# Kernel optimization log

Hardware: AMD Instinct MI355X
Metric: run time of the kernel (lower is better)

## Reference

```python
import jax, jax.numpy as jnp
import numpy as np

B, T = 64, 256
STOCH, DETER = 1024, 4096
D = 512          # attention_dim == embed_dim == heads*dim_head
H, HD = 8, 64    # heads, dim_head
FF = 2 * D       # feedforward hidden
L = 2            # transformer layers
NT = 255         # embedding rows (len(targets))
OUT = 255        # np.prod(shape)
SCALE = HD ** -0.5
EPS = 1e-5


def _ln(x, g, b):
    m = jnp.mean(x, axis=-1, keepdims=True)
    v = jnp.mean((x - m) ** 2, axis=-1, keepdims=True)
    return (x - m) * jax.lax.rsqrt(v + EPS) * g + b


def setup_inputs() -> dict:
    key = jax.random.key(0)
    ks = jax.random.split(key, 32)
    r = lambda i, shp, s=0.02: (jax.random.normal(ks[i], shp, dtype=jnp.float32) * s)
    inp = {
        'stoch': jax.random.normal(ks[0], (B, T, STOCH), dtype=jnp.float32),
        'deter': jax.random.normal(ks[1], (B, T, DETER), dtype=jnp.float32),
        'targets_array': jax.random.randint(ks[2], (B, T), 0, NT),
        'emb': r(3, (NT, D), 1.0),
        'Ws': r(4, (D, STOCH)), 'bs': jnp.zeros((D,), jnp.float32),
        'Wd': r(5, (D, DETER)), 'bd': jnp.zeros((D,), jnp.float32),
        # per-layer stacked params [L, ...]
        'ln1_g': jnp.ones((L, D), jnp.float32), 'ln1_b': jnp.zeros((L, D), jnp.float32),
        'Wqkv': r(6, (L, 3 * H * HD, D)),
        'Wout': r(7, (L, D, H * HD)), 'bout': jnp.zeros((L, D), jnp.float32),
        'ln2_g': jnp.ones((L, D), jnp.float32), 'ln2_b': jnp.zeros((L, D), jnp.float32),
        'W1': r(8, (L, FF, D)), 'b1': jnp.zeros((L, FF), jnp.float32),
        'W2': r(9, (L, D, FF)), 'b2': jnp.zeros((L, D), jnp.float32),
        'W1b': r(10, (L, FF, D)), 'b1b': jnp.zeros((L, FF), jnp.float32),
        'W2b': r(11, (L, D, FF)), 'b2b': jnp.zeros((L, D), jnp.float32),
        'Wm': r(12, (OUT, D)), 'bm': jnp.zeros((OUT,), jnp.float32),
    }
    return inp


def _forward(stoch, deter, targets_array, emb, Ws, bs, Wd, bd,
             ln1_g, ln1_b, Wqkv, Wout, bout, ln2_g, ln2_b,
             W1, b1, W2, b2, W1b, b1b, W2b, b2b, Wm, bm):
    N = B * T
    s = stoch.reshape(N, STOCH)
    d = deter.reshape(N, DETER)
    tg = targets_array.reshape(N)
    tok1 = (s @ Ws.T + bs)[:, None, :]   # [N,1,D]
    tok2 = (d @ Wd.T + bd)[:, None, :]
    x = jnp.concatenate([tok1, tok2], axis=1)   # [N,2,D]
    q2 = emb[tg][:, None, :]                    # [N,1,D]

    for l in range(L):
        # PreNorm -> Attention (residuals connect to the normalized inputs,
        # exactly as in the original code)
        xn = _ln(x, ln1_g[l], ln1_b[l])
        qn = _ln(q2, ln1_g[l], ln1_b[l])
        qkv = xn @ Wqkv[l].T                            # [N,2,3*H*HD]
        q, k, v = jnp.split(qkv, 3, axis=-1)
        q = q.reshape(N, 2, H, HD).transpose(0, 2, 1, 3)   # [N,H,2,HD]
        k = k.reshape(N, 2, H, HD).transpose(0, 2, 1, 3)
        v = v.reshape(N, 2, H, HD).transpose(0, 2, 1, 3)
        qq2 = qn.reshape(N, 1, H, HD).transpose(0, 2, 1, 3)  # [N,H,1,HD]
        dots = jnp.einsum('nhqd,nhkd->nhqk', q, k) * SCALE
        dots2 = jnp.einsum('nhqd,nhkd->nhqk', qq2, k) * SCALE
        attn = jax.nn.log_softmax(dots, axis=-1)    # LogSoftmax attention!
        attn2 = jax.nn.log_softmax(dots2, axis=-1)
        out = jnp.einsum('nhqk,nhkd->nhqd', attn, v).transpose(0, 2, 1, 3).reshape(N, 2, H * HD)
        qout = jnp.einsum('nhqk,nhkd->nhqd', attn2, v).transpose(0, 2, 1, 3).reshape(N, 1, H * HD)
        x = out @ Wout[l].T + bout[l] + xn   # to_out on self stream only
        q2 = qout + qn                        # cross stream has NO projection

        # PreNorm -> FeedForward (dual streams, separate MLPs, exact GELU)
        xn = _ln(x, ln2_g[l], ln2_b[l])
        qn = _ln(q2, ln2_g[l], ln2_b[l])
        x = jax.nn.gelu(xn @ W1[l].T + b1[l], approximate=False) @ W2[l].T + b2[l] + xn
        q2 = jax.nn.gelu(qn @ W1b[l].T + b1b[l], approximate=False) @ W2b[l].T + b2b[l] + qn

    out = q2.reshape(B, T, D)
    mean = out @ Wm.T + bm   # [B,T,OUT]
    return mean


def reference(stoch, deter, targets_array, emb, Ws, bs, Wd, bd,
              ln1_g, ln1_b, Wqkv, Wout, bout, ln2_g, ln2_b,
              W1, b1, W2, b2, W1b, b1b, W2b, b2b, Wm, bm):
    return _forward(stoch, deter, targets_array, emb, Ws, bs, Wd, bd,
                    ln1_g, ln1_b, Wqkv, Wout, bout, ln2_g, ln2_b,
                    W1, b1, W2, b2, W1b, b1b, W2b, b2b, Wm, bm)
```

## Files before the change

### kernel.cpp

```cpp
#include <hip/hip_runtime.h>
#include <cstdint>
#include <cstddef>


#define NTOK   16384
#define TWO_N  32768
#define DMODEL 512
#define HEADS  8
#define HDIM   64
#define FFDIM  1024
#define KSTOCH 1024
#define KDETER 4096
#define QKVD   1536
#define NOUT   255

typedef short bf16x8 __attribute__((ext_vector_type(8)));
typedef float f32x4  __attribute__((ext_vector_type(4)));

__device__ inline unsigned short bfbits(float f) {
  union { float f; unsigned u; } x; x.f = f;
  unsigned r = x.u + 0x7fffu + ((x.u >> 16) & 1u);
  return (unsigned short)(r >> 16);
}
__device__ inline float bf2f(unsigned short s) {
  union { unsigned u; float f; } x; x.u = ((unsigned)s) << 16;
  return x.f;
}
__device__ inline float wave_sum(float v) {
  #pragma unroll
  for (int o = 32; o > 0; o >>= 1) v += __shfl_xor(v, o);
  return v;
}

struct CvtEnt { const float* src; unsigned short* dst; int n4; int ntot4; };
struct CvtArgs { CvtEnt e[11]; };

__global__ __launch_bounds__(256) void cvt_kernel(CvtArgs args) {
  CvtEnt ent = args.e[blockIdx.y];
  int stride = gridDim.x * 256;
  for (int i = blockIdx.x * 256 + threadIdx.x; i < ent.ntot4; i += stride) {
    float4 v;
    if (i < ent.n4) v = ((const float4*)ent.src)[i];
    else            v = make_float4(0.f, 0.f, 0.f, 0.f);
    ushort4 o;
    o.x = bfbits(v.x); o.y = bfbits(v.y); o.z = bfbits(v.z); o.w = bfbits(v.w);
    ((ushort4*)ent.dst)[i] = o;
  }
}

__global__ __launch_bounds__(128) void gather_kernel(
    const float* __restrict__ emb, const int* __restrict__ tg,
    float* __restrict__ q2) {
  int n = blockIdx.x;
  int row = tg[n];
  ((float4*)(q2 + (size_t)n * DMODEL))[threadIdx.x] =
      ((const float4*)(emb + (size_t)row * DMODEL))[threadIdx.x];
}

__global__ __launch_bounds__(256) void ln_kernel(
    const float* __restrict__ x, const float* __restrict__ g,
    const float* __restrict__ b, float* __restrict__ of,
    unsigned short* __restrict__ ob, int rows) {
  int w = threadIdx.x >> 6, l = threadIdx.x & 63;
  long row = (long)blockIdx.x * 4 + w;
  if (row >= rows) return;
  const float* xr = x + row * DMODEL;
  float4 v0 = ((const float4*)xr)[l];
  float4 v1 = ((const float4*)xr)[l + 64];
  float s  = v0.x + v0.y + v0.z + v0.w + v1.x + v1.y + v1.z + v1.w;
  float ss = v0.x*v0.x + v0.y*v0.y + v0.z*v0.z + v0.w*v0.w
           + v1.x*v1.x + v1.y*v1.y + v1.z*v1.z + v1.w*v1.w;
  s = wave_sum(s); ss = wave_sum(ss);
  float mean = s * (1.f / DMODEL);
  float var  = ss * (1.f / DMODEL) - mean * mean;
  float r = rsqrtf(var + 1e-5f);

  float4 g0 = ((const float4*)g)[l],      b0 = ((const float4*)b)[l];
  float4 g1 = ((const float4*)g)[l + 64], b1 = ((const float4*)b)[l + 64];
  float4 o0, o1;
  o0.x = (v0.x - mean) * r * g0.x + b0.x;  o0.y = (v0.y - mean) * r * g0.y + b0.y;
  o0.z = (v0.z - mean) * r * g0.z + b0.z;  o0.w = (v0.w - mean) * r * g0.w + b0.w;
  o1.x = (v1.x - mean) * r * g1.x + b1.x;  o1.y = (v1.y - mean) * r * g1.y + b1.y;
  o1.z = (v1.z - mean) * r * g1.z + b1.z;  o1.w = (v1.w - mean) * r * g1.w + b1.w;
  float* ofr = of + row * DMODEL;
  ((float4*)ofr)[l] = o0; ((float4*)ofr)[l + 64] = o1;
  unsigned short* obr = ob + row * DMODEL;
  ushort4 p0, p1;
  p0.x = bfbits(o0.x); p0.y = bfbits(o0.y); p0.z = bfbits(o0.z); p0.w = bfbits(o0.w);
  p1.x = bfbits(o1.x); p1.y = bfbits(o1.y); p1.z = bfbits(o1.z); p1.w = bfbits(o1.w);
  ((ushort4*)obr)[l] = p0; ((ushort4*)obr)[l + 64] = p1;
}

__global__ __launch_bounds__(256) void attn_kernel(
    const unsigned short* __restrict__ qkv, const unsigned short* __restrict__ qnb,
    const float* __restrict__ qnf, float* __restrict__ q2,
    unsigned short* __restrict__ attnout) {
  int w = threadIdx.x >> 6, l = threadIdx.x & 63;
  int idx = blockIdx.x * 4 + w;
  int n = idx >> 3, h = idx & 7;
  const unsigned short* r0 = qkv + (size_t)(2 * n) * QKVD + h * HDIM + l;
  float q0 = bf2f(r0[0]),     k0 = bf2f(r0[512]),      v0 = bf2f(r0[1024]);
  float q1 = bf2f(r0[QKVD]),  k1 = bf2f(r0[QKVD+512]), v1 = bf2f(r0[QKVD+1024]);
  size_t qoff = (size_t)n * DMODEL + h * HDIM + l;
  float qq = bf2f(qnb[qoff]);

  float d00 = q0*k0, d01 = q0*k1, d10 = q1*k0, d11 = q1*k1, e0 = qq*k0, e1 = qq*k1;
  #pragma unroll
  for (int o = 32; o > 0; o >>= 1) {
    d00 += __shfl_xor(d00, o); d01 += __shfl_xor(d01, o);
    d10 += __shfl_xor(d10, o); d11 += __shfl_xor(d11, o);
    e0  += __shfl_xor(e0, o);  e1  += __shfl_xor(e1, o);
  }
  const float SC = 0.125f;
  d00 *= SC; d01 *= SC; d10 *= SC; d11 *= SC; e0 *= SC; e1 *= SC;
  auto lsm2 = [](float& a, float& b) {
    float m = fmaxf(a, b);
    float lse = m + logf(expf(a - m) + expf(b - m));
    a -= lse; b -= lse;
  };
  lsm2(d00, d01); lsm2(d10, d11); lsm2(e0, e1);

  float o0 = d00 * v0 + d01 * v1;
  float o1 = d10 * v0 + d11 * v1;
  float oq = e0 * v0 + e1 * v1;
  attnout[(size_t)(2 * n)     * DMODEL + h * HDIM + l] = bfbits(o0);
  attnout[(size_t)(2 * n + 1) * DMODEL + h * HDIM + l] = bfbits(o1);
  q2[qoff] = oq + qnf[qoff];
}

template <bool GELU>
__global__ __launch_bounds__(256, 2) void gemm_kernel(
    const unsigned short* __restrict__ A, const unsigned short* __restrict__ B,
    const float* __restrict__ bias, const float* __restrict__ res,
    float* __restrict__ Cf, unsigned short* __restrict__ Cb,
    int M, int Nvalid, int K, int ldc, int ldcb, int ldres, int ntn) {
  __shared__ short lsA[128 * 64];
  __shared__ short lsB[128 * 64];
  int tm = blockIdx.x / ntn, tn = blockIdx.x % ntn;
  int tid = threadIdx.x;
  int w = tid >> 6, l = tid & 63;
  int wr = w >> 1, wc = w & 1;

  int srow = w * 32 + (l >> 3);
  int scol = (l & 7) * 8;
  const unsigned short* ga = A + (size_t)(tm * 128 + srow) * K + scol;
  const unsigned short* gb = B + (size_t)(tn * 128 + srow) * K + scol;
  short* la = lsA + w * 2048;
  short* lb = lsB + w * 2048;

  f32x4 acc[4][4] = {};

  for (int k0 = 0; k0 < K; k0 += 64) {
    #pragma unroll
    for (int r = 0; r < 4; ++r) {
      __builtin_amdgcn_global_load_lds(
          (const __attribute__((address_space(1))) void*)(ga + k0 + (size_t)r * 8 * K),
          (__attribute__((address_space(3))) void*)(la + r * 512), 16, 0, 0);
      __builtin_amdgcn_global_load_lds(
          (const __attribute__((address_space(1))) void*)(gb + k0 + (size_t)r * 8 * K),
          (__attribute__((address_space(3))) void*)(lb + r * 512), 16, 0, 0);
    }
    __syncthreads();
    #pragma unroll
    for (int kk = 0; kk < 2; ++kk) {
      bf16x8 af[4], bfr[4];
      #pragma unroll
      for (int i = 0; i < 4; ++i)
        af[i] = *(const bf16x8*)(lsA + (wr * 64 + i * 16 + (l & 15)) * 64 +
                                 kk * 32 + (l >> 4) * 8);
      #pragma unroll
      for (int i = 0; i < 4; ++i)
        bfr[i] = *(const bf16x8*)(lsB + (wc * 64 + i * 16 + (l & 15)) * 64 +
                                  kk * 32 + (l >> 4) * 8);
      #pragma unroll
      for (int mi = 0; mi < 4; ++mi)
        #pragma unroll
        for (int ni = 0; ni < 4; ++ni)
          acc[mi][ni] = __builtin_amdgcn_mfma_f32_16x16x32_bf16(
              af[mi], bfr[ni], acc[mi][ni], 0, 0, 0);
    }
    __syncthreads();
  }

  int lr = l >> 4, lc = l & 15;
  #pragma unroll
  for (int mi = 0; mi < 4; ++mi) {
    #pragma unroll
    for (int ni = 0; ni < 4; ++ni) {
      int gn = tn * 128 + wc * 64 + ni * 16 + lc;
      bool okn = gn < Nvalid;
      float bv = (bias != nullptr && okn) ? bias[gn] : 0.f;
      f32x4 a = acc[mi][ni];
      #pragma unroll
      for (int j = 0; j < 4; ++j) {
        int gm = tm * 128 + wr * 64 + mi * 16 + lr * 4 + j;
        float v = a[j] + bv;
        if (GELU) v = 0.5f * v * (1.f + erff(v * 0.70710678118654752f));
        if (okn) {
          if (res) v += res[(size_t)gm * ldres + gn];
          if (Cf) Cf[(size_t)gm * ldc + gn] = v;
          if (Cb) Cb[(size_t)gm * ldcb + gn] = bfbits(v);
        }
      }
    }
  }
}

extern "C" void kernel_launch(void* const* d_in, const int* in_sizes, int n_in,
                              void* d_out, int out_size, void* d_ws, size_t ws_size,
                              hipStream_t stream) {
  const float* stoch = (const float*)d_in[0];
  const float* deter = (const float*)d_in[1];
  const int*   tg    = (const int*)d_in[2];
  const float* emb   = (const float*)d_in[3];
  const float* Ws    = (const float*)d_in[4];
  const float* bs    = (const float*)d_in[5];
  const float* Wd    = (const float*)d_in[6];
  const float* bd    = (const float*)d_in[7];
  const float* ln1g  = (const float*)d_in[8];
  const float* ln1b  = (const float*)d_in[9];
  const float* Wqkv  = (const float*)d_in[10];
  const float* Wout  = (const float*)d_in[11];
  const float* bout  = (const float*)d_in[12];
  const float* ln2g  = (const float*)d_in[13];
  const float* ln2b  = (const float*)d_in[14];
  const float* W1    = (const float*)d_in[15];
  const float* b1    = (const float*)d_in[16];
  const float* W2    = (const float*)d_in[17];
  const float* b2    = (const float*)d_in[18];
  const float* W1b   = (const float*)d_in[19];
  const float* b1b   = (const float*)d_in[20];
  const float* W2b   = (const float*)d_in[21];
  const float* b2b   = (const float*)d_in[22];
  const float* Wm    = (const float*)d_in[23];
  const float* bm    = (const float*)d_in[24];
  float* out = (float*)d_out;

  char* p = (char*)d_ws;
  size_t off = 0;
  auto alloc = [&](size_t bytes) {
    void* r = p + off;
    off += (bytes + 255) & ~(size_t)255;
    return r;
  };
  unsigned short* s_bf = (unsigned short*)alloc((size_t)NTOK * KSTOCH * 2);
  unsigned short* d_bf = (unsigned short*)alloc((size_t)NTOK * KDETER * 2);
  float* x    = (float*)alloc((size_t)TWO_N * DMODEL * 4);
  float* q2   = (float*)alloc((size_t)NTOK * DMODEL * 4);
  float* xnf  = (float*)alloc((size_t)TWO_N * DMODEL * 4);
  float* qnf  = (float*)alloc((size_t)NTOK * DMODEL * 4);
  unsigned short* xnb  = (unsigned short*)alloc((size_t)TWO_N * DMODEL * 2);
  unsigned short* qnb  = (unsigned short*)alloc((size_t)NTOK * DMODEL * 2);
  unsigned short* qkvb = (unsigned short*)alloc((size_t)TWO_N * QKVD * 2);
  unsigned short* Wsb   = (unsigned short*)alloc((size_t)DMODEL * KSTOCH * 2);
  unsigned short* Wdb   = (unsigned short*)alloc((size_t)DMODEL * KDETER * 2);
  unsigned short* Wqkvb = (unsigned short*)alloc((size_t)2 * QKVD * DMODEL * 2);
  unsigned short* Woutb = (unsigned short*)alloc((size_t)2 * DMODEL * DMODEL * 2);
  unsigned short* W1bf  = (unsigned short*)alloc((size_t)2 * FFDIM * DMODEL * 2);
  unsigned short* W2bf  = (unsigned short*)alloc((size_t)2 * DMODEL * FFDIM * 2);
  unsigned short* W1bbf = (unsigned short*)alloc((size_t)2 * FFDIM * DMODEL * 2);
  unsigned short* W2bbf = (unsigned short*)alloc((size_t)2 * DMODEL * FFDIM * 2);
  unsigned short* Wmb   = (unsigned short*)alloc((size_t)256 * DMODEL * 2);
  unsigned short* attnout = s_bf;
  unsigned short* q2b     = d_bf;
  unsigned short* hb      = qkvb;
  unsigned short* hqb     = qkvb + (size_t)TWO_N * FFDIM;

  CvtArgs ca;
  ca.e[0]  = { stoch, s_bf,  NTOK * KSTOCH / 4,  NTOK * KSTOCH / 4 };
  ca.e[1]  = { deter, d_bf,  NTOK * KDETER / 4,  NTOK * KDETER / 4 };
  ca.e[2]  = { Ws,    Wsb,   DMODEL * KSTOCH / 4, DMODEL * KSTOCH / 4 };
  ca.e[3]  = { Wd,    Wdb,   DMODEL * KDETER / 4, DMODEL * KDETER / 4 };
  ca.e[4]  = { Wqkv,  Wqkvb, 2 * QKVD * DMODEL / 4, 2 * QKVD * DMODEL / 4 };
  ca.e[5]  = { Wout,  Woutb, 2 * DMODEL * DMODEL / 4, 2 * DMODEL * DMODEL / 4 };
  ca.e[6]  = { W1,    W1bf,  2 * FFDIM * DMODEL / 4, 2 * FFDIM * DMODEL / 4 };
  ca.e[7]  = { W2,    W2bf,  2 * DMODEL * FFDIM / 4, 2 * DMODEL * FFDIM / 4 };
  ca.e[8]  = { W1b,   W1bbf, 2 * FFDIM * DMODEL / 4, 2 * FFDIM * DMODEL / 4 };
  ca.e[9]  = { W2b,   W2bbf, 2 * DMODEL * FFDIM / 4, 2 * DMODEL * FFDIM / 4 };
  ca.e[10] = { Wm,    Wmb,   NOUT * DMODEL / 4,   256 * DMODEL / 4 };
  cvt_kernel<<<dim3(1024, 11), 256, 0, stream>>>(ca);

  gemm_kernel<false><<<128 * 4, 256, 0, stream>>>(
      s_bf, Wsb, bs, nullptr, x, nullptr, NTOK, DMODEL, KSTOCH, 2 * DMODEL, 0, 0, 4);
  gemm_kernel<false><<<128 * 4, 256, 0, stream>>>(
      d_bf, Wdb, bd, nullptr, x + DMODEL, nullptr, NTOK, DMODEL, KDETER, 2 * DMODEL, 0, 0, 4);

  gather_kernel<<<NTOK, 128, 0, stream>>>(emb, tg, q2);

  for (int l = 0; l < 2; ++l) {
    ln_kernel<<<TWO_N / 4, 256, 0, stream>>>(x, ln1g + 512 * l, ln1b + 512 * l, xnf, xnb, TWO_N);
    ln_kernel<<<NTOK / 4, 256, 0, stream>>>(q2, ln1g + 512 * l, ln1b + 512 * l, qnf, qnb, NTOK);
    gemm_kernel<false><<<256 * 12, 256, 0, stream>>>(
        xnb, Wqkvb + (size_t)l * QKVD * DMODEL, nullptr, nullptr, nullptr, qkvb,
        TWO_N, QKVD, DMODEL, 0, QKVD, 0, 12);
    attn_kernel<<<NTOK * HEADS / 4, 256, 0, stream>>>(qkvb, qnb, qnf, q2, attnout);
    gemm_kernel<false><<<256 * 4, 256, 0, stream>>>(
        attnout, Woutb + (size_t)l * DMODEL * DMODEL, bout + 512 * l, xnf, x, nullptr,
        TWO_N, DMODEL, DMODEL, DMODEL, 0, DMODEL, 4);
    ln_kernel<<<TWO_N / 4, 256, 0, stream>>>(x, ln2g + 512 * l, ln2b + 512 * l, xnf, xnb, TWO_N);
    ln_kernel<<<NTOK / 4, 256, 0, stream>>>(q2, ln2g + 512 * l, ln2b + 512 * l, qnf, qnb, NTOK);
    gemm_kernel<true><<<256 * 8, 256, 0, stream>>>(
        xnb, W1bf + (size_t)l * FFDIM * DMODEL, b1 + 1024 * l, nullptr, nullptr, hb,
        TWO_N, FFDIM, DMODEL, 0, FFDIM, 0, 8);
    gemm_kernel<false><<<256 * 4, 256, 0, stream>>>(
        hb, W2bf + (size_t)l * DMODEL * FFDIM, b2 + 512 * l, xnf, x, nullptr,
        TWO_N, DMODEL, FFDIM, DMODEL, 0, DMODEL, 4);
    gemm_kernel<true><<<128 * 8, 256, 0, stream>>>(
        qnb, W1bbf + (size_t)l * FFDIM * DMODEL, b1b + 1024 * l, nullptr, nullptr, hqb,
        NTOK, FFDIM, DMODEL, 0, FFDIM, 0, 8);
    gemm_kernel<false><<<128 * 4, 256, 0, stream>>>(
        hqb, W2bbf + (size_t)l * DMODEL * FFDIM, b2b + 512 * l, qnf, q2, q2b,
        NTOK, DMODEL, FFDIM, DMODEL, DMODEL, DMODEL, 4);
  }

  gemm_kernel<false><<<128 * 2, 256, 0, stream>>>(
      q2b, Wmb, bm, nullptr, out, nullptr, NTOK, NOUT, DMODEL, NOUT, 0, 0, 2);

  (void)in_sizes; (void)n_in; (void)out_size; (void)ws_size;
}
```

Measured before the change: 2.101 ms.

## Merge LayerNorm launches, drop fp32 normed copies, remap GEMM blocks across XCDs

Merges the two LayerNorm launches per norm into one kernel covering both streams, and drops the fp32 normalized output so residuals are read back from the bf16 copy. This removes fp32 stores and loads in the LN, attention and GEMM epilogues. The GEMM also remaps block IDs so consecutive tiles land on the same XCD for better L2 reuse, and raises min blocks per CU from 2 to 3. The bf16 residual loses precision, and the tighter launch bound may cause register spills.

```diff
diff --git a/kernel.cpp b/kernel.cpp
--- a/kernel.cpp
+++ b/kernel.cpp
@@ -57,16 +57,24 @@
       ((const float4*)(emb + (size_t)row * DMODEL))[threadIdx.x];
 }
 
-__global__ __launch_bounds__(256) void ln_kernel(
-    const float* __restrict__ x, const float* __restrict__ g,
-    const float* __restrict__ b, float* __restrict__ of,
-    unsigned short* __restrict__ ob, int rows) {
+__global__ __launch_bounds__(256) void ln2_kernel(
+    const float* __restrict__ xs, const float* __restrict__ qs,
+    const float* __restrict__ g, const float* __restrict__ b,
+    unsigned short* __restrict__ xb, unsigned short* __restrict__ qb) {
   int w = threadIdx.x >> 6, l = threadIdx.x & 63;
-  long row = (long)blockIdx.x * 4 + w;
-  if (row >= rows) return;
-  const float* xr = x + row * DMODEL;
-  float4 v0 = ((const float4*)xr)[l];
-  float4 v1 = ((const float4*)xr)[l + 64];
+  int row = blockIdx.x * 4 + w;
+  const float* src;
+  unsigned short* dst;
+  if (row < TWO_N) {
+    src = xs + (size_t)row * DMODEL;
+    dst = xb + (size_t)row * DMODEL;
+  } else {
+    int r2 = row - TWO_N;
+    src = qs + (size_t)r2 * DMODEL;
+    dst = qb + (size_t)r2 * DMODEL;
+  }
+  float4 v0 = ((const float4*)src)[l];
+  float4 v1 = ((const float4*)src)[l + 64];
   float s  = v0.x + v0.y + v0.z + v0.w + v1.x + v1.y + v1.z + v1.w;
   float ss = v0.x*v0.x + v0.y*v0.y + v0.z*v0.z + v0.w*v0.w
            + v1.x*v1.x + v1.y*v1.y + v1.z*v1.z + v1.w*v1.w;
@@ -77,24 +85,21 @@
 
   float4 g0 = ((const float4*)g)[l],      b0 = ((const float4*)b)[l];
   float4 g1 = ((const float4*)g)[l + 64], b1 = ((const float4*)b)[l + 64];
-  float4 o0, o1;
-  o0.x = (v0.x - mean) * r * g0.x + b0.x;  o0.y = (v0.y - mean) * r * g0.y + b0.y;
-  o0.z = (v0.z - mean) * r * g0.z + b0.z;  o0.w = (v0.w - mean) * r * g0.w + b0.w;
-  o1.x = (v1.x - mean) * r * g1.x + b1.x;  o1.y = (v1.y - mean) * r * g1.y + b1.y;
-  o1.z = (v1.z - mean) * r * g1.z + b1.z;  o1.w = (v1.w - mean) * r * g1.w + b1.w;
-  float* ofr = of + row * DMODEL;
-  ((float4*)ofr)[l] = o0; ((float4*)ofr)[l + 64] = o1;
-  unsigned short* obr = ob + row * DMODEL;
   ushort4 p0, p1;
-  p0.x = bfbits(o0.x); p0.y = bfbits(o0.y); p0.z = bfbits(o0.z); p0.w = bfbits(o0.w);
-  p1.x = bfbits(o1.x); p1.y = bfbits(o1.y); p1.z = bfbits(o1.z); p1.w = bfbits(o1.w);
-  ((ushort4*)obr)[l] = p0; ((ushort4*)obr)[l + 64] = p1;
+  p0.x = bfbits((v0.x - mean) * r * g0.x + b0.x);
+  p0.y = bfbits((v0.y - mean) * r * g0.y + b0.y);
+  p0.z = bfbits((v0.z - mean) * r * g0.z + b0.z);
+  p0.w = bfbits((v0.w - mean) * r * g0.w + b0.w);
+  p1.x = bfbits((v1.x - mean) * r * g1.x + b1.x);
+  p1.y = bfbits((v1.y - mean) * r * g1.y + b1.y);
+  p1.z = bfbits((v1.z - mean) * r * g1.z + b1.z);
+  p1.w = bfbits((v1.w - mean) * r * g1.w + b1.w);
+  ((ushort4*)dst)[l] = p0; ((ushort4*)dst)[l + 64] = p1;
 }
 
 __global__ __launch_bounds__(256) void attn_kernel(
     const unsigned short* __restrict__ qkv, const unsigned short* __restrict__ qnb,
-    const float* __restrict__ qnf, float* __restrict__ q2,
-    unsigned short* __restrict__ attnout) {
+    float* __restrict__ q2, unsigned short* __restrict__ attnout) {
   int w = threadIdx.x >> 6, l = threadIdx.x & 63;
   int idx = blockIdx.x * 4 + w;
   int n = idx >> 3, h = idx & 7;
@@ -125,18 +130,22 @@
   float oq = e0 * v0 + e1 * v1;
   attnout[(size_t)(2 * n)     * DMODEL + h * HDIM + l] = bfbits(o0);
   attnout[(size_t)(2 * n + 1) * DMODEL + h * HDIM + l] = bfbits(o1);
-  q2[qoff] = oq + qnf[qoff];
+  q2[qoff] = oq + qq;
 }
 
 template <bool GELU>
-__global__ __launch_bounds__(256, 2) void gemm_kernel(
+__global__ __launch_bounds__(256, 3) void gemm_kernel(
     const unsigned short* __restrict__ A, const unsigned short* __restrict__ B,
-    const float* __restrict__ bias, const float* __restrict__ res,
+    const float* __restrict__ bias, const unsigned short* __restrict__ res,
     float* __restrict__ Cf, unsigned short* __restrict__ Cb,
     int M, int Nvalid, int K, int ldc, int ldcb, int ldres, int ntn) {
   __shared__ short lsA[128 * 64];
   __shared__ short lsB[128 * 64];
-  int tm = blockIdx.x / ntn, tn = blockIdx.x % ntn;
+  int nwg = gridDim.x;
+  int q8 = nwg >> 3, r8 = nwg & 7;
+  int xcd = blockIdx.x & 7, lin = blockIdx.x >> 3;
+  int bid = (xcd < r8 ? xcd * (q8 + 1) : r8 * (q8 + 1) + (xcd - r8) * q8) + lin;
+  int tm = bid / ntn, tn = bid % ntn;
   int tid = threadIdx.x;
   int w = tid >> 6, l = tid & 63;
   int wr = w >> 1, wc = w & 1;
@@ -197,7 +206,7 @@
         float v = a[j] + bv;
         if (GELU) v = 0.5f * v * (1.f + erff(v * 0.70710678118654752f));
         if (okn) {
-          if (res) v += res[(size_t)gm * ldres + gn];
+          if (res) v += bf2f(res[(size_t)gm * ldres + gn]);
           if (Cf) Cf[(size_t)gm * ldc + gn] = v;
           if (Cb) Cb[(size_t)gm * ldcb + gn] = bfbits(v);
         }
@@ -247,8 +256,6 @@
   unsigned short* d_bf = (unsigned short*)alloc((size_t)NTOK * KDETER * 2);
   float* x    = (float*)alloc((size_t)TWO_N * DMODEL * 4);
   float* q2   = (float*)alloc((size_t)NTOK * DMODEL * 4);
-  float* xnf  = (float*)alloc((size_t)TWO_N * DMODEL * 4);
-  float* qnf  = (float*)alloc((size_t)NTOK * DMODEL * 4);
   unsigned short* xnb  = (unsigned short*)alloc((size_t)TWO_N * DMODEL * 2);
   unsigned short* qnb  = (unsigned short*)alloc((size_t)NTOK * DMODEL * 2);
   unsigned short* qkvb = (unsigned short*)alloc((size_t)TWO_N * QKVD * 2);
@@ -287,29 +294,28 @@
 
   gather_kernel<<<NTOK, 128, 0, stream>>>(emb, tg, q2);
 
+  const int LN_GRID = (TWO_N + NTOK) / 4;
   for (int l = 0; l < 2; ++l) {
-    ln_kernel<<<TWO_N / 4, 256, 0, stream>>>(x, ln1g + 512 * l, ln1b + 512 * l, xnf, xnb, TWO_N);
-    ln_kernel<<<NTOK / 4, 256, 0, stream>>>(q2, ln1g + 512 * l, ln1b + 512 * l, qnf, qnb, NTOK);
+    ln2_kernel<<<LN_GRID, 256, 0, stream>>>(x, q2, ln1g + 512 * l, ln1b + 512 * l, xnb, qnb);
     gemm_kernel<false><<<256 * 12, 256, 0, stream>>>(
         xnb, Wqkvb + (size_t)l * QKVD * DMODEL, nullptr, nullptr, nullptr, qkvb,
         TWO_N, QKVD, DMODEL, 0, QKVD, 0, 12);
-    attn_kernel<<<NTOK * HEADS / 4, 256, 0, stream>>>(qkvb, qnb, qnf, q2, attnout);
+    attn_kernel<<<NTOK * HEADS / 4, 256, 0, stream>>>(qkvb, qnb, q2, attnout);
     gemm_kernel<false><<<256 * 4, 256, 0, stream>>>(
-        attnout, Woutb + (size_t)l * DMODEL * DMODEL, bout + 512 * l, xnf, x, nullptr,
+        attnout, Woutb + (size_t)l * DMODEL * DMODEL, bout + 512 * l, xnb, x, nullptr,
         TWO_N, DMODEL, DMODEL, DMODEL, 0, DMODEL, 4);
-    ln_kernel<<<TWO_N / 4, 256, 0, stream>>>(x, ln2g + 512 * l, ln2b + 512 * l, xnf, xnb, TWO_N);
-    ln_kernel<<<NTOK / 4, 256, 0, stream>>>(q2, ln2g + 512 * l, ln2b + 512 * l, qnf, qnb, NTOK);
+    ln2_kernel<<<LN_GRID, 256, 0, stream>>>(x, q2, ln2g + 512 * l, ln2b + 512 * l, xnb, qnb);
     gemm_kernel<true><<<256 * 8, 256, 0, stream>>>(
         xnb, W1bf + (size_t)l * FFDIM * DMODEL, b1 + 1024 * l, nullptr, nullptr, hb,
         TWO_N, FFDIM, DMODEL, 0, FFDIM, 0, 8);
     gemm_kernel<false><<<256 * 4, 256, 0, stream>>>(
-        hb, W2bf + (size_t)l * DMODEL * FFDIM, b2 + 512 * l, xnf, x, nullptr,
+        hb, W2bf + (size_t)l * DMODEL * FFDIM, b2 + 512 * l, xnb, x, nullptr,
         TWO_N, DMODEL, FFDIM, DMODEL, 0, DMODEL, 4);
     gemm_kernel<true><<<128 * 8, 256, 0, stream>>>(
         qnb, W1bbf + (size_t)l * FFDIM * DMODEL, b1b + 1024 * l, nullptr, nullptr, hqb,
         NTOK, FFDIM, DMODEL, 0, FFDIM, 0, 8);
     gemm_kernel<false><<<128 * 4, 256, 0, stream>>>(
-        hqb, W2bbf + (size_t)l * DMODEL * FFDIM, b2b + 512 * l, qnf, q2, q2b,
+        hqb, W2bbf + (size_t)l * DMODEL * FFDIM, b2b + 512 * l, qnb, q2, q2b,
         NTOK, DMODEL, FFDIM, DMODEL, DMODEL, DMODEL, 4);
   }
 
```

Result: faster. 1.810 ms (-13.9%).
